# Kernel tuning notes

Hardware: AMD Instinct MI355X
Metric: run time of the kernel (lower is better)

The kernel has to match this reference:

```python
import jax, jax.numpy as jnp
import numpy as np

N = 100000      # nodes
E = 1600000     # edges
D_IN = 32
D_OUT = 32
K = 2           # propagation hops; module has k+1 alpha scalars


def setup_inputs() -> dict:
    key = jax.random.key(0)
    k1, k2, k3, k4, k5 = jax.random.split(key, 5)
    feat = jax.random.normal(k1, (N, D_IN), dtype=jnp.float32)
    src = jax.random.randint(k2, (E,), 0, N, dtype=jnp.int32)
    dst = jax.random.randint(k3, (E,), 0, N, dtype=jnp.int32)
    stdv = 1.0 / np.sqrt(D_OUT)
    W = jax.random.uniform(k4, (D_OUT, D_IN), dtype=jnp.float32, minval=-stdv, maxval=stdv)
    b = jnp.zeros((D_OUT,), dtype=jnp.float32)
    stdvk = 1.0 / np.sqrt(K)
    alpha = jax.random.uniform(k5, (K + 1,), dtype=jnp.float32, minval=-stdvk, maxval=stdvk)
    return {"feat": feat, "src": src, "dst": dst, "W": W, "b": b, "alpha": alpha}


def reference(feat, src, dst, W, b, alpha):
    n = feat.shape[0]
    # in-degrees (edges point src -> dst; copy_u/sum aggregates at dst)
    deg = jax.ops.segment_sum(jnp.ones_like(dst, dtype=jnp.float32), dst, num_segments=n)
    norm = jnp.maximum(deg, 1.0)[:, None] ** -0.5  # [n,1]

    feats = [feat]
    h = feat
    for _ in range(K):
        h = h * norm                                       # pre-normalize
        h = jax.ops.segment_sum(h[src], dst, num_segments=n)  # SpMM: gather+scatter-add
        h = h * norm                                       # post-normalize
        feats.append(h)

    # result = sum_i fc(alpha_i * feat_i); bias added once per hop term (as in torch)
    result = jnp.zeros((n, W.shape[0]), dtype=jnp.float32)
    for i, f in enumerate(feats):
        result = result + (alpha[i] * f) @ W.T + b
    return result
```

## Files before the change

### kernel.cpp

```cpp
#include <hip/hip_runtime.h>

#define D 32
#define CHUNK 8192
#define BWID 256
#define BSH 8
#define NBCAP 512
#define EBCAP 6144
#define SCAN_T 256
#define SCAN_V 4
#define SCAN_CHUNK 1024

__device__ __forceinline__ unsigned f2bf2(float lo, float hi) {
    union { float f; unsigned u; } a, b;
    a.f = lo; b.f = hi;
    unsigned ra = a.u + 0x7FFFu + ((a.u >> 16) & 1u);
    unsigned rb = b.u + 0x7FFFu + ((b.u >> 16) & 1u);
    return (ra >> 16) | (rb & 0xFFFF0000u);
}
__device__ __forceinline__ void bf2_unpack(unsigned u, float& lo, float& hi) {
    union { unsigned u; float f; } a, b;
    a.u = u << 16; b.u = u & 0xFFFF0000u;
    lo = a.f; hi = b.f;
}


__global__ void p1_count_kernel(const int* __restrict__ dst, int* __restrict__ cnt,
                                int E, int NB) {
    __shared__ int h[NBCAP];
    int blk = blockIdx.x, t = threadIdx.x;
    for (int i = t; i < NB; i += 256) h[i] = 0;
    __syncthreads();
    int base = blk * CHUNK;
    int end = min(base + CHUNK, E);
    for (int a = base + t * 4; a < end; a += 1024) {
        if (a + 3 < end) {
            int4 d = *(const int4*)(dst + a);
            atomicAdd(&h[d.x >> BSH], 1);
            atomicAdd(&h[d.y >> BSH], 1);
            atomicAdd(&h[d.z >> BSH], 1);
            atomicAdd(&h[d.w >> BSH], 1);
        } else {
            for (int e = a; e < end && e < a + 4; ++e) atomicAdd(&h[dst[e] >> BSH], 1);
        }
    }
    __syncthreads();
    for (int i = t; i < NB; i += 256) cnt[(size_t)blk * NB + i] = h[i];
}

__global__ void red_kernel(const int* __restrict__ cnt, int* __restrict__ btot,
                           int GB, int NB) {
    __shared__ int s[256];
    int b = blockIdx.x, t = threadIdx.x;
    int acc = 0;
    for (int g = t; g < GB; g += 256) acc += cnt[(size_t)g * NB + b];
    s[t] = acc;
    __syncthreads();
    for (int off = 128; off > 0; off >>= 1) {
        if (t < off) s[t] += s[t + off];
        __syncthreads();
    }
    if (t == 0) btot[b] = s[0];
}

__global__ void scanb_kernel(const int* __restrict__ btot, int* __restrict__ bbase, int NB) {
    __shared__ int s[256];
    __shared__ int carry;
    int t = threadIdx.x;
    if (t == 0) carry = 0;
    __syncthreads();
    for (int base = 0; base < NB; base += 256) {
        int v = (base + t < NB) ? btot[base + t] : 0;
        s[t] = v;
        __syncthreads();
        for (int off = 1; off < 256; off <<= 1) {
            int x = (t >= off) ? s[t - off] : 0;
            __syncthreads();
            s[t] += x;
            __syncthreads();
        }
        if (base + t < NB) bbase[base + t] = carry + s[t] - v;
        __syncthreads();
        if (t == 255) carry += s[255];
        __syncthreads();
    }
    if (t == 0) bbase[NB] = carry;
}

__global__ void off_kernel(const int* __restrict__ cnt, const int* __restrict__ bbase,
                           int* __restrict__ off, int GB, int NB) {
    __shared__ int st[256];
    int b = blockIdx.x, t = threadIdx.x;
    int g0 = 2 * t, g1 = 2 * t + 1;
    int c0 = (g0 < GB) ? cnt[(size_t)g0 * NB + b] : 0;
    int c1 = (g1 < GB) ? cnt[(size_t)g1 * NB + b] : 0;
    int pair = c0 + c1;
    st[t] = pair;
    __syncthreads();
    for (int o = 1; o < 256; o <<= 1) {
        int x = (t >= o) ? st[t - o] : 0;
        __syncthreads();
        st[t] += x;
        __syncthreads();
    }
    int ex = bbase[b] + st[t] - pair;
    if (g0 < GB) off[(size_t)g0 * NB + b] = ex;
    if (g1 < GB) off[(size_t)g1 * NB + b] = ex + c0;
}

__global__ void p3_scatter_kernel(const int* __restrict__ src, const int* __restrict__ dst,
                                  const int* __restrict__ off, unsigned* __restrict__ ebuf,
                                  int E, int NB) {
    __shared__ int cur[NBCAP];
    int blk = blockIdx.x, t = threadIdx.x;
    for (int i = t; i < NB; i += 256) cur[i] = off[(size_t)blk * NB + i];
    __syncthreads();
    int base = blk * CHUNK;
    int end = min(base + CHUNK, E);
    for (int a = base + t * 4; a < end; a += 1024) {
        if (a + 3 < end) {
            int4 d = *(const int4*)(dst + a);
            int4 s = *(const int4*)(src + a);
            int p0 = atomicAdd(&cur[d.x >> BSH], 1);
            int p1 = atomicAdd(&cur[d.y >> BSH], 1);
            int p2 = atomicAdd(&cur[d.z >> BSH], 1);
            int p3 = atomicAdd(&cur[d.w >> BSH], 1);
            ebuf[p0] = ((unsigned)(d.x & (BWID - 1)) << 23) | (unsigned)s.x;
            ebuf[p1] = ((unsigned)(d.y & (BWID - 1)) << 23) | (unsigned)s.y;
            ebuf[p2] = ((unsigned)(d.z & (BWID - 1)) << 23) | (unsigned)s.z;
            ebuf[p3] = ((unsigned)(d.w & (BWID - 1)) << 23) | (unsigned)s.w;
        } else {
            for (int e = a; e < end && e < a + 4; ++e) {
                int dv = dst[e];
                int p = atomicAdd(&cur[dv >> BSH], 1);
                ebuf[p] = ((unsigned)(dv & (BWID - 1)) << 23) | (unsigned)src[e];
            }
        }
    }
}

__global__ void p4_kernel(const unsigned* __restrict__ ebuf, const int* __restrict__ bbase,
                          int* __restrict__ row_start, int* __restrict__ row_end,
                          float* __restrict__ norm, int* __restrict__ csr_src,
                          const float4* __restrict__ feat4, uint4* __restrict__ A1q, int N) {
    __shared__ unsigned eb[EBCAP];
    __shared__ int deg2[BWID];
    __shared__ int rs[BWID];
    __shared__ int st[256];
    int b = blockIdx.x, t = threadIdx.x;
    int node0 = b << BSH;
    int nn = min(BWID, N - node0);
    int e0 = bbase[b], e1 = bbase[b + 1];
    int ne = e1 - e0;
    bool staged = (ne <= EBCAP);

    if (t < BWID) deg2[t] = 0;
    __syncthreads();
    if (staged) {
        for (int j = t; j < ne; j += 256) {
            unsigned v = ebuf[e0 + j];
            eb[j] = v;
            atomicAdd(&deg2[v >> 23], 1);
        }
    } else {
        for (int j = t; j < ne; j += 256)
            atomicAdd(&deg2[ebuf[e0 + j] >> 23], 1);
    }
    __syncthreads();
    int dg = deg2[t];
    st[t] = dg;
    __syncthreads();
    for (int off = 1; off < 256; off <<= 1) {
        int v = (t >= off) ? st[t - off] : 0;
        __syncthreads();
        st[t] += v;
        __syncthreads();
    }
    int ex = st[t] - dg;
    rs[t] = ex;
    if (t < nn) {
        row_start[node0 + t] = e0 + ex;
        row_end[node0 + t]   = e0 + ex + dg;
        norm[node0 + t] = rsqrtf(fmaxf((float)dg, 1.0f));
    }
    __syncthreads();
    if (staged) {
        for (int j = t; j < ne; j += 256) {
            unsigned v = eb[j];
            int p = atomicAdd(&rs[v >> 23], 1);
            csr_src[e0 + p] = (int)(v & 0x7FFFFF);
        }
    } else {
        for (int j = t; j < ne; j += 256) {
            unsigned v = ebuf[e0 + j];
            int p = atomicAdd(&rs[v >> 23], 1);
            csr_src[e0 + p] = (int)(v & 0x7FFFFF);
        }
    }
    for (int c = t; c < nn * 4; c += 256) {
        int nl = c >> 2, q = c & 3;
        float nv = rsqrtf(fmaxf((float)deg2[nl], 1.0f));
        size_t rf = (size_t)(node0 + nl) * 8 + q * 2;
        float4 f0 = feat4[rf], f1 = feat4[rf + 1];
        uint4 o;
        o.x = f2bf2(f0.x * nv, f0.y * nv);
        o.y = f2bf2(f0.z * nv, f0.w * nv);
        o.z = f2bf2(f1.x * nv, f1.y * nv);
        o.w = f2bf2(f1.z * nv, f1.w * nv);
        A1q[(size_t)(node0 + nl) * 4 + q] = o;
    }
}

__global__ void degpos_kernel(const int* __restrict__ dst, int* __restrict__ deg,
                              int* __restrict__ pos, int E) {
    int t = blockIdx.x * blockDim.x + threadIdx.x;
    int base = t * 4;
    if (base + 3 < E) {
        int4 d = *(const int4*)(dst + base);
        int4 p;
        p.x = atomicAdd(&deg[d.x], 1);
        p.y = atomicAdd(&deg[d.y], 1);
        p.z = atomicAdd(&deg[d.z], 1);
        p.w = atomicAdd(&deg[d.w], 1);
        *(int4*)(pos + base) = p;
    } else if (base < E) {
        for (int e = base; e < E; ++e) pos[e] = atomicAdd(&deg[dst[e]], 1);
    }
}

__global__ void scan1_kernel(const int* __restrict__ deg, int* __restrict__ partial, int n) {
    __shared__ int sdata[SCAN_T];
    int base = blockIdx.x * SCAN_CHUNK + threadIdx.x * SCAN_V;
    int s = 0;
    #pragma unroll
    for (int k = 0; k < SCAN_V; ++k) { int i = base + k; if (i < n) s += deg[i]; }
    sdata[threadIdx.x] = s;
    __syncthreads();
    for (int off = SCAN_T / 2; off > 0; off >>= 1) {
        if (threadIdx.x < off) sdata[threadIdx.x] += sdata[threadIdx.x + off];
        __syncthreads();
    }
    if (threadIdx.x == 0) partial[blockIdx.x] = sdata[0];
}

__global__ void scan2_kernel(int* __restrict__ partial, int nb) {
    __shared__ int sdata[256];
    int v = (threadIdx.x < nb) ? partial[threadIdx.x] : 0;
    sdata[threadIdx.x] = v;
    __syncthreads();
    for (int off = 1; off < 256; off <<= 1) {
        int t = (threadIdx.x >= off) ? sdata[threadIdx.x - off] : 0;
        __syncthreads();
        sdata[threadIdx.x] += t;
        __syncthreads();
    }
    if (threadIdx.x < nb) partial[threadIdx.x] = sdata[threadIdx.x] - v;
}

__global__ void scan3_kernel(const int* __restrict__ deg, const int* __restrict__ partial,
                             int* __restrict__ row_start, int* __restrict__ row_end,
                             float* __restrict__ norm, int n) {
    __shared__ int sdata[SCAN_T];
    int base = blockIdx.x * SCAN_CHUNK + threadIdx.x * SCAN_V;
    int v[SCAN_V];
    int s = 0;
    #pragma unroll
    for (int k = 0; k < SCAN_V; ++k) { int i = base + k; v[k] = (i < n) ? deg[i] : 0; s += v[k]; }
    int self = s;
    sdata[threadIdx.x] = s;
    __syncthreads();
    for (int off = 1; off < SCAN_T; off <<= 1) {
        int t = (threadIdx.x >= off) ? sdata[threadIdx.x - off] : 0;
        __syncthreads();
        sdata[threadIdx.x] += t;
        __syncthreads();
    }
    int run = partial[blockIdx.x] + sdata[threadIdx.x] - self;
    #pragma unroll
    for (int k = 0; k < SCAN_V; ++k) {
        int i = base + k;
        if (i < n) {
            row_start[i] = run;
            row_end[i]   = run + v[k];
            norm[i] = rsqrtf(fmaxf((float)v[k], 1.0f));
            run += v[k];
        }
    }
}

__global__ void fillA_kernel(const int* __restrict__ src, const int* __restrict__ dst,
                             const int* __restrict__ pos, const int* __restrict__ row_start,
                             int* __restrict__ csr_src, int E) {
    int t = blockIdx.x * blockDim.x + threadIdx.x;
    int base = t * 4;
    if (base + 3 < E) {
        int4 d = *(const int4*)(dst + base);
        int4 p = *(const int4*)(pos + base);
        int4 s = *(const int4*)(src + base);
        csr_src[row_start[d.x] + p.x] = s.x;
        csr_src[row_start[d.y] + p.y] = s.y;
        csr_src[row_start[d.z] + p.z] = s.z;
        csr_src[row_start[d.w] + p.w] = s.w;
    } else if (base < E) {
        for (int e = base; e < E; ++e)
            csr_src[row_start[dst[e]] + pos[e]] = src[e];
    }
}

__global__ void prep_kernel(const float4* __restrict__ feat4, const float* __restrict__ norm,
                            uint4* __restrict__ A1q, int nchunk) {
    int i = blockIdx.x * blockDim.x + threadIdx.x;
    if (i >= nchunk) return;
    int v = i >> 2;
    float nv = norm[v];
    float4 f0 = feat4[(size_t)i * 2], f1 = feat4[(size_t)i * 2 + 1];
    uint4 o;
    o.x = f2bf2(f0.x * nv, f0.y * nv);
    o.y = f2bf2(f0.z * nv, f0.w * nv);
    o.z = f2bf2(f1.x * nv, f1.y * nv);
    o.w = f2bf2(f1.z * nv, f1.w * nv);
    A1q[i] = o;
}

#define ACC_EDGE(V)                                              \
    { float lo_, hi_;                                            \
      bf2_unpack((V).x, lo_, hi_); acc[0] += lo_; acc[1] += hi_; \
      bf2_unpack((V).y, lo_, hi_); acc[2] += lo_; acc[3] += hi_; \
      bf2_unpack((V).z, lo_, hi_); acc[4] += lo_; acc[5] += hi_; \
      bf2_unpack((V).w, lo_, hi_); acc[6] += lo_; acc[7] += hi_; }

__global__ __launch_bounds__(256) void gather1_kernel(
        const int* __restrict__ row_start, const int* __restrict__ row_end,
        const int* __restrict__ csr_src, const uint4* __restrict__ A1q,
        const float4* __restrict__ feat4, const float* __restrict__ norm,
        const float* __restrict__ alpha, float4* __restrict__ G,
        uint4* __restrict__ A2q, int n) {
    int wave = blockIdx.x * (blockDim.x >> 6) + (threadIdx.x >> 6);
    int lane = threadIdx.x & 63;
    int g  = lane >> 4;
    int eo = (lane >> 2) & 3;
    int q  = lane & 3;
    int r = wave * 4 + g;
    int s0 = 0, e1 = 0;
    if (r < n) { s0 = row_start[r]; e1 = row_end[r]; }
    float acc[8];
    #pragma unroll
    for (int i = 0; i < 8; ++i) acc[i] = 0.f;
    int j = s0 + eo;
    for (; j + 4 < e1; j += 8) {
        int sa = csr_src[j];
        int sb = csr_src[j + 4];
        uint4 va = A1q[(size_t)sa * 4 + q];
        uint4 vb = A1q[(size_t)sb * 4 + q];
        ACC_EDGE(va);
        ACC_EDGE(vb);
    }
    if (j < e1) {
        int sa = csr_src[j];
        uint4 va = A1q[(size_t)sa * 4 + q];
        ACC_EDGE(va);
    }
    #pragma unroll
    for (int i = 0; i < 8; ++i) {
        acc[i] += __shfl_xor(acc[i], 4);
        acc[i] += __shfl_xor(acc[i], 8);
    }
    if (eo == 0 && r < n) {
        float nv = norm[r];
        float a0 = alpha[0], a1 = alpha[1];
        size_t rf = (size_t)r * 8 + q * 2;
        float4 f0 = feat4[rf], f1 = feat4[rf + 1];
        float h[8];
        #pragma unroll
        for (int i = 0; i < 8; ++i) h[i] = acc[i] * nv;
        G[rf]     = make_float4(fmaf(a1, h[0], a0 * f0.x), fmaf(a1, h[1], a0 * f0.y),
                                fmaf(a1, h[2], a0 * f0.z), fmaf(a1, h[3], a0 * f0.w));
        G[rf + 1] = make_float4(fmaf(a1, h[4], a0 * f1.x), fmaf(a1, h[5], a0 * f1.y),
                                fmaf(a1, h[6], a0 * f1.z), fmaf(a1, h[7], a0 * f1.w));
        uint4 o;
        o.x = f2bf2(h[0] * nv, h[1] * nv);
        o.y = f2bf2(h[2] * nv, h[3] * nv);
        o.z = f2bf2(h[4] * nv, h[5] * nv);
        o.w = f2bf2(h[6] * nv, h[7] * nv);
        A2q[(size_t)r * 4 + q] = o;
    }
}

__global__ __launch_bounds__(256) void gather2_kernel(
        const int* __restrict__ row_start, const int* __restrict__ row_end,
        const int* __restrict__ csr_src, const uint4* __restrict__ A2q,
        const float* __restrict__ norm, const float* __restrict__ alpha,
        const float* __restrict__ W, const float* __restrict__ b,
        float4* __restrict__ G, int n) {
    __shared__ float Wl[D][D + 1];
    __shared__ float pbuf[4][4][D];
    int tid = threadIdx.x;
    for (int k = tid; k < D * D; k += 256) Wl[k >> 5][k & 31] = W[k];
    __syncthreads();

    int wv = tid >> 6;
    int wave = blockIdx.x * 4 + wv;
    int lane = tid & 63;
    int g  = lane >> 4;
    int eo = (lane >> 2) & 3;
    int q  = lane & 3;
    int r = wave * 4 + g;
    int s0 = 0, e1 = 0;
    if (r < n) { s0 = row_start[r]; e1 = row_end[r]; }
    float acc[8];
    #pragma unroll
    for (int i = 0; i < 8; ++i) acc[i] = 0.f;
    int j = s0 + eo;
    for (; j + 4 < e1; j += 8) {
        int sa = csr_src[j];
        int sb = csr_src[j + 4];
        uint4 va = A2q[(size_t)sa * 4 + q];
        uint4 vb = A2q[(size_t)sb * 4 + q];
        ACC_EDGE(va);
        ACC_EDGE(vb);
    }
    if (j < e1) {
        int sa = csr_src[j];
        uint4 va = A2q[(size_t)sa * 4 + q];
        ACC_EDGE(va);
    }
    #pragma unroll
    for (int i = 0; i < 8; ++i) {
        acc[i] += __shfl_xor(acc[i], 4);
        acc[i] += __shfl_xor(acc[i], 8);
    }
    if (eo == 0 && r < n) {
        float nv = norm[r];
        float a2 = alpha[2];
        size_t rf = (size_t)r * 8 + q * 2;
        float4 g0 = G[rf], g1 = G[rf + 1];
        float4 p0 = make_float4(fmaf(a2, acc[0] * nv, g0.x), fmaf(a2, acc[1] * nv, g0.y),
                                fmaf(a2, acc[2] * nv, g0.z), fmaf(a2, acc[3] * nv, g0.w));
        float4 p1 = make_float4(fmaf(a2, acc[4] * nv, g1.x), fmaf(a2, acc[5] * nv, g1.y),
                                fmaf(a2, acc[6] * nv, g1.z), fmaf(a2, acc[7] * nv, g1.w));
        *(float4*)&pbuf[wv][g][q * 8]     = p0;
        *(float4*)&pbuf[wv][g][q * 8 + 4] = p1;
    }
    asm volatile("s_waitcnt lgkmcnt(0)" ::: "memory");

    int o  = lane & 31;
    int rr = lane >> 5;
    #pragma unroll
    for (int rp = 0; rp < 2; ++rp) {
        int gg = rp * 2 + rr;
        int row = wave * 4 + gg;
        if (row < n) {
            float acco = 0.f;
            #pragma unroll
            for (int k = 0; k < D; ++k)
                acco = fmaf(pbuf[wv][gg][k], Wl[o][k], acco);
            ((float*)G)[(size_t)row * D + o] = acco + 3.0f * b[o];
        }
    }
}

extern "C" void kernel_launch(void* const* d_in, const int* in_sizes, int n_in,
                              void* d_out, int out_size, void* d_ws, size_t ws_size,
                              hipStream_t stream) {
    const float* feat  = (const float*)d_in[0];
    const int*   src   = (const int*)  d_in[1];
    const int*   dst   = (const int*)  d_in[2];
    const float* W     = (const float*)d_in[3];
    const float* b     = (const float*)d_in[4];
    const float* alpha = (const float*)d_in[5];

    const int N  = in_sizes[0] / D;
    const int E  = in_sizes[1];
    const int BT = 256;
    const int NB = (N + BWID - 1) >> BSH;
    const int GB = (E + CHUNK - 1) / CHUNK;
    const int gblocks = (N + 15) / 16;
    float4* G = (float4*)d_out;

    size_t needA = ((size_t)32 * N + 2 * (size_t)GB * NB + 2 * NB + 1
                    + 2 * (size_t)E + 3 * (size_t)N) * 4;

    if (ws_size >= needA && NB <= NBCAP && GB <= 512 && N < (1 << 23)) {
        unsigned* A1q       = (unsigned*)d_ws;
        unsigned* A2q       = A1q + (size_t)16 * N;
        int*      cnt       = (int*)(A2q + (size_t)16 * N);
        int*      off       = cnt + (size_t)GB * NB;
        int*      btot      = off + (size_t)GB * NB;
        int*      bbase     = btot + NB;
        unsigned* ebuf      = (unsigned*)(bbase + NB + 1);
        int*      csr_src   = (int*)(ebuf + E);
        int*      row_start = csr_src + E;
        int*      row_end   = row_start + N;
        float*    norm      = (float*)(row_end + N);

        p1_count_kernel<<<GB, BT, 0, stream>>>(dst, cnt, E, NB);
        red_kernel<<<NB, BT, 0, stream>>>(cnt, btot, GB, NB);
        scanb_kernel<<<1, BT, 0, stream>>>(btot, bbase, NB);
        off_kernel<<<NB, BT, 0, stream>>>(cnt, bbase, off, GB, NB);
        p3_scatter_kernel<<<GB, BT, 0, stream>>>(src, dst, off, ebuf, E, NB);
        p4_kernel<<<NB, BT, 0, stream>>>(ebuf, bbase, row_start, row_end, norm, csr_src,
                                         (const float4*)feat, (uint4*)A1q, N);
        gather1_kernel<<<gblocks, BT, 0, stream>>>(row_start, row_end, csr_src,
                                                   (const uint4*)A1q, (const float4*)feat,
                                                   norm, alpha, G, (uint4*)A2q, N);
        gather2_kernel<<<gblocks, BT, 0, stream>>>(row_start, row_end, csr_src,
                                                   (const uint4*)A2q, norm, alpha,
                                                   W, b, G, N);
    } else {
        const int nb = (N + SCAN_CHUNK - 1) / SCAN_CHUNK;
        const int e4blocks = ((E + 3) / 4 + BT - 1) / BT;
        unsigned* A1q       = (unsigned*)d_ws;
        unsigned* A2q       = A1q + (size_t)16 * N;
        int*      deg       = (int*)(A2q + (size_t)16 * N);
        int*      pos       = deg + N;
        int*      partial   = pos + E;
        int*      row_start = partial + 256;
        int*      row_end   = row_start + N;
        int*      csr_src   = row_end + N;
        float*    norm      = (float*)(csr_src + E);

        hipMemsetAsync(deg, 0, (size_t)N * sizeof(int), stream);
        degpos_kernel<<<e4blocks, BT, 0, stream>>>(dst, deg, pos, E);
        scan1_kernel<<<nb, SCAN_T, 0, stream>>>(deg, partial, N);
        scan2_kernel<<<1, 256, 0, stream>>>(partial, nb);
        scan3_kernel<<<nb, SCAN_T, 0, stream>>>(deg, partial, row_start, row_end, norm, N);
        fillA_kernel<<<e4blocks, BT, 0, stream>>>(src, dst, pos, row_start, csr_src, E);
        prep_kernel<<<(4 * N + BT - 1) / BT, BT, 0, stream>>>(
            (const float4*)feat, norm, (uint4*)A1q, 4 * N);
        gather1_kernel<<<gblocks, BT, 0, stream>>>(row_start, row_end, csr_src,
                                                   (const uint4*)A1q, (const float4*)feat,
                                                   norm, alpha, G, (uint4*)A2q, N);
        gather2_kernel<<<gblocks, BT, 0, stream>>>(row_start, row_end, csr_src,
                                                   (const uint4*)A2q, norm, alpha,
                                                   W, b, G, N);
    }
}
```

Measured before the change: 106.6 us.

## Sort rows by degree within blocks for gather load balance and unroll edge loop

Within each 256-node bucket, p4 builds a permutation that orders nodes by in-degree (capped at 63) with a small counting sort. Both gather kernels then process rows through this permutation, so the four rows sharing a wave have similar edge counts and less time is lost waiting on the longest row. The edge loops are also unrolled to keep four independent gathers in flight instead of two. The permutation costs an extra indirection per row and makes reads of row_start, feat and G less contiguous; the fallback path fills it with the identity.

```diff
diff --git a/kernel.cpp b/kernel.cpp
--- a/kernel.cpp
+++ b/kernel.cpp
@@ -141,11 +141,13 @@
 __global__ void p4_kernel(const unsigned* __restrict__ ebuf, const int* __restrict__ bbase,
                           int* __restrict__ row_start, int* __restrict__ row_end,
                           float* __restrict__ norm, int* __restrict__ csr_src,
-                          const float4* __restrict__ feat4, uint4* __restrict__ A1q, int N) {
+                          const float4* __restrict__ feat4, uint4* __restrict__ A1q,
+                          int* __restrict__ perm, int N) {
     __shared__ unsigned eb[EBCAP];
     __shared__ int deg2[BWID];
     __shared__ int rs[BWID];
     __shared__ int st[256];
+    __shared__ int bins[64];
     int b = blockIdx.x, t = threadIdx.x;
     int node0 = b << BSH;
     int nn = min(BWID, N - node0);
@@ -154,6 +156,7 @@
     bool staged = (ne <= EBCAP);
 
     if (t < BWID) deg2[t] = 0;
+    if (t < 64) bins[t] = 0;
     __syncthreads();
     if (staged) {
         for (int j = t; j < ne; j += 256) {
@@ -195,6 +198,18 @@
             int p = atomicAdd(&rs[v >> 23], 1);
             csr_src[e0 + p] = (int)(v & 0x7FFFFF);
         }
+    }
+    int key = min(dg, 63);
+    if (t < nn) atomicAdd(&bins[key], 1);
+    __syncthreads();
+    if (t == 0) {
+        int run = 0;
+        for (int k = 0; k < 64; ++k) { int c = bins[k]; bins[k] = run; run += c; }
+    }
+    __syncthreads();
+    if (t < nn) {
+        int p = atomicAdd(&bins[key], 1);
+        perm[node0 + p] = node0 + t;
     }
     for (int c = t; c < nn * 4; c += 256) {
         int nl = c >> 2, q = c & 3;
@@ -258,7 +273,7 @@
 
 __global__ void scan3_kernel(const int* __restrict__ deg, const int* __restrict__ partial,
                              int* __restrict__ row_start, int* __restrict__ row_end,
-                             float* __restrict__ norm, int n) {
+                             float* __restrict__ norm, int* __restrict__ perm, int n) {
     __shared__ int sdata[SCAN_T];
     int base = blockIdx.x * SCAN_CHUNK + threadIdx.x * SCAN_V;
     int v[SCAN_V];
@@ -282,6 +297,7 @@
             row_start[i] = run;
             row_end[i]   = run + v[k];
             norm[i] = rsqrtf(fmaxf((float)v[k], 1.0f));
+            perm[i] = i;
             run += v[k];
         }
     }
@@ -332,29 +348,32 @@
         const int* __restrict__ row_start, const int* __restrict__ row_end,
         const int* __restrict__ csr_src, const uint4* __restrict__ A1q,
         const float4* __restrict__ feat4, const float* __restrict__ norm,
-        const float* __restrict__ alpha, float4* __restrict__ G,
-        uint4* __restrict__ A2q, int n) {
+        const float* __restrict__ alpha, const int* __restrict__ perm,
+        float4* __restrict__ G, uint4* __restrict__ A2q, int n) {
     int wave = blockIdx.x * (blockDim.x >> 6) + (threadIdx.x >> 6);
     int lane = threadIdx.x & 63;
     int g  = lane >> 4;
     int eo = (lane >> 2) & 3;
     int q  = lane & 3;
-    int r = wave * 4 + g;
-    int s0 = 0, e1 = 0;
-    if (r < n) { s0 = row_start[r]; e1 = row_end[r]; }
+    int slot = wave * 4 + g;
+    int r = -1, s0 = 0, e1 = 0;
+    if (slot < n) { r = perm[slot]; s0 = row_start[r]; e1 = row_end[r]; }
     float acc[8];
     #pragma unroll
     for (int i = 0; i < 8; ++i) acc[i] = 0.f;
     int j = s0 + eo;
-    for (; j + 4 < e1; j += 8) {
-        int sa = csr_src[j];
-        int sb = csr_src[j + 4];
-        uint4 va = A1q[(size_t)sa * 4 + q];
-        uint4 vb = A1q[(size_t)sb * 4 + q];
-        ACC_EDGE(va);
-        ACC_EDGE(vb);
-    }
-    if (j < e1) {
+    for (; j + 12 < e1; j += 16) {
+        int i0 = csr_src[j];
+        int i1 = csr_src[j + 4];
+        int i2 = csr_src[j + 8];
+        int i3 = csr_src[j + 12];
+        uint4 v0 = A1q[(size_t)i0 * 4 + q];
+        uint4 v1 = A1q[(size_t)i1 * 4 + q];
+        uint4 v2 = A1q[(size_t)i2 * 4 + q];
+        uint4 v3 = A1q[(size_t)i3 * 4 + q];
+        ACC_EDGE(v0); ACC_EDGE(v1); ACC_EDGE(v2); ACC_EDGE(v3);
+    }
+    for (; j < e1; j += 4) {
         int sa = csr_src[j];
         uint4 va = A1q[(size_t)sa * 4 + q];
         ACC_EDGE(va);
@@ -364,7 +383,7 @@
         acc[i] += __shfl_xor(acc[i], 4);
         acc[i] += __shfl_xor(acc[i], 8);
     }
-    if (eo == 0 && r < n) {
+    if (eo == 0 && r >= 0) {
         float nv = norm[r];
         float a0 = alpha[0], a1 = alpha[1];
         size_t rf = (size_t)r * 8 + q * 2;
@@ -390,7 +409,7 @@
         const int* __restrict__ csr_src, const uint4* __restrict__ A2q,
         const float* __restrict__ norm, const float* __restrict__ alpha,
         const float* __restrict__ W, const float* __restrict__ b,
-        float4* __restrict__ G, int n) {
+        const int* __restrict__ perm, float4* __restrict__ G, int n) {
     __shared__ float Wl[D][D + 1];
     __shared__ float pbuf[4][4][D];
     int tid = threadIdx.x;
@@ -403,22 +422,25 @@
     int g  = lane >> 4;
     int eo = (lane >> 2) & 3;
     int q  = lane & 3;
-    int r = wave * 4 + g;
-    int s0 = 0, e1 = 0;
-    if (r < n) { s0 = row_start[r]; e1 = row_end[r]; }
+    int slot = wave * 4 + g;
+    int r = -1, s0 = 0, e1 = 0;
+    if (slot < n) { r = perm[slot]; s0 = row_start[r]; e1 = row_end[r]; }
     float acc[8];
     #pragma unroll
     for (int i = 0; i < 8; ++i) acc[i] = 0.f;
     int j = s0 + eo;
-    for (; j + 4 < e1; j += 8) {
-        int sa = csr_src[j];
-        int sb = csr_src[j + 4];
-        uint4 va = A2q[(size_t)sa * 4 + q];
-        uint4 vb = A2q[(size_t)sb * 4 + q];
-        ACC_EDGE(va);
-        ACC_EDGE(vb);
-    }
-    if (j < e1) {
+    for (; j + 12 < e1; j += 16) {
+        int i0 = csr_src[j];
+        int i1 = csr_src[j + 4];
+        int i2 = csr_src[j + 8];
+        int i3 = csr_src[j + 12];
+        uint4 v0 = A2q[(size_t)i0 * 4 + q];
+        uint4 v1 = A2q[(size_t)i1 * 4 + q];
+        uint4 v2 = A2q[(size_t)i2 * 4 + q];
+        uint4 v3 = A2q[(size_t)i3 * 4 + q];
+        ACC_EDGE(v0); ACC_EDGE(v1); ACC_EDGE(v2); ACC_EDGE(v3);
+    }
+    for (; j < e1; j += 4) {
         int sa = csr_src[j];
         uint4 va = A2q[(size_t)sa * 4 + q];
         ACC_EDGE(va);
@@ -428,7 +450,7 @@
         acc[i] += __shfl_xor(acc[i], 4);
         acc[i] += __shfl_xor(acc[i], 8);
     }
-    if (eo == 0 && r < n) {
+    if (eo == 0 && r >= 0) {
         float nv = norm[r];
         float a2 = alpha[2];
         size_t rf = (size_t)r * 8 + q * 2;
@@ -447,8 +469,9 @@
     #pragma unroll
     for (int rp = 0; rp < 2; ++rp) {
         int gg = rp * 2 + rr;
-        int row = wave * 4 + gg;
-        if (row < n) {
+        int gslot = wave * 4 + gg;
+        if (gslot < n) {
+            int row = perm[gslot];
             float acco = 0.f;
             #pragma unroll
             for (int k = 0; k < D; ++k)
@@ -477,7 +500,7 @@
     float4* G = (float4*)d_out;
 
     size_t needA = ((size_t)32 * N + 2 * (size_t)GB * NB + 2 * NB + 1
-                    + 2 * (size_t)E + 3 * (size_t)N) * 4;
+                    + 2 * (size_t)E + 4 * (size_t)N) * 4;
 
     if (ws_size >= needA && NB <= NBCAP && GB <= 512 && N < (1 << 23)) {
         unsigned* A1q       = (unsigned*)d_ws;
@@ -491,6 +514,7 @@
         int*      row_start = csr_src + E;
         int*      row_end   = row_start + N;
         float*    norm      = (float*)(row_end + N);
+        int*      perm      = (int*)(norm + N);
 
         p1_count_kernel<<<GB, BT, 0, stream>>>(dst, cnt, E, NB);
         red_kernel<<<NB, BT, 0, stream>>>(cnt, btot, GB, NB);
@@ -498,13 +522,13 @@
         off_kernel<<<NB, BT, 0, stream>>>(cnt, bbase, off, GB, NB);
         p3_scatter_kernel<<<GB, BT, 0, stream>>>(src, dst, off, ebuf, E, NB);
         p4_kernel<<<NB, BT, 0, stream>>>(ebuf, bbase, row_start, row_end, norm, csr_src,
-                                         (const float4*)feat, (uint4*)A1q, N);
+                                         (const float4*)feat, (uint4*)A1q, perm, N);
         gather1_kernel<<<gblocks, BT, 0, stream>>>(row_start, row_end, csr_src,
                                                    (const uint4*)A1q, (const float4*)feat,
-                                                   norm, alpha, G, (uint4*)A2q, N);
+                                                   norm, alpha, perm, G, (uint4*)A2q, N);
         gather2_kernel<<<gblocks, BT, 0, stream>>>(row_start, row_end, csr_src,
                                                    (const uint4*)A2q, norm, alpha,
-                                                   W, b, G, N);
+                                                   W, b, perm, G, N);
     } else {
         const int nb = (N + SCAN_CHUNK - 1) / SCAN_CHUNK;
         const int e4blocks = ((E + 3) / 4 + BT - 1) / BT;
@@ -517,20 +541,21 @@
         int*      row_end   = row_start + N;
         int*      csr_src   = row_end + N;
         float*    norm      = (float*)(csr_src + E);
+        int*      perm      = (int*)(norm + N);
 
         hipMemsetAsync(deg, 0, (size_t)N * sizeof(int), stream);
         degpos_kernel<<<e4blocks, BT, 0, stream>>>(dst, deg, pos, E);
         scan1_kernel<<<nb, SCAN_T, 0, stream>>>(deg, partial, N);
         scan2_kernel<<<1, 256, 0, stream>>>(partial, nb);
-        scan3_kernel<<<nb, SCAN_T, 0, stream>>>(deg, partial, row_start, row_end, norm, N);
+        scan3_kernel<<<nb, SCAN_T, 0, stream>>>(deg, partial, row_start, row_end, norm, perm, N);
         fillA_kernel<<<e4blocks, BT, 0, stream>>>(src, dst, pos, row_start, csr_src, E);
         prep_kernel<<<(4 * N + BT - 1) / BT, BT, 0, stream>>>(
             (const float4*)feat, norm, (uint4*)A1q, 4 * N);
         gather1_kernel<<<gblocks, BT, 0, stream>>>(row_start, row_end, csr_src,
                                                    (const uint4*)A1q, (const float4*)feat,
-                                                   norm, alpha, G, (uint4*)A2q, N);
+                                                   norm, alpha, perm, G, (uint4*)A2q, N);
         gather2_kernel<<<gblocks, BT, 0, stream>>>(row_start, row_end, csr_src,
                                                    (const uint4*)A2q, norm, alpha,
-                                                   W, b, G, N);
-    }
-}
+                                                   W, b, perm, G, N);
+    }
+}
```

Measured after the change: 116.9 us. +9.7%, slower.
